# Kernel optimization log

Measured on AMD Instinct MI355X. Metric: run time of the kernel, lower is better.

The kernel has to match this reference:

```python
import jax, jax.numpy as jnp
import numpy as np

D_MODEL = 128
N_HEADS = 8
N_POINTS = 8
MAX_RES = 10.0


def setup_inputs() -> dict:
    key = jax.random.key(0)
    ks = jax.random.split(key, 12)
    B, C, H, W = 4, D_MODEL, 128, 128
    nh, P = N_HEADS, N_POINTS
    inp = {
        'nbr_fea': jax.random.normal(ks[0], (B, C, H, W), jnp.float32),
        'ext_fea': jax.random.normal(ks[1], (B, C, H, W), jnp.float32),
        'flow': jax.random.normal(ks[2], (B, 2, H, W), jnp.float32) * 2.0,
        'W_off': jax.random.normal(ks[3], (C, nh * P * 2), jnp.float32) * 0.02,
        'b_off': jax.random.normal(ks[4], (nh * P * 2,), jnp.float32) * 0.02,
        'W_attn': jax.random.normal(ks[5], (C, nh * P), jnp.float32) * 0.02,
        'b_attn': jnp.zeros((nh * P,), jnp.float32),
        'W_val': jax.random.normal(ks[6], (C, C), jnp.float32) * (1.0 / np.sqrt(C)),
        'b_val': jnp.zeros((C,), jnp.float32),
        'W_out': jax.random.normal(ks[7], (C, C), jnp.float32) * (1.0 / np.sqrt(C)),
        'b_out': jnp.zeros((C,), jnp.float32),
    }
    return inp


def _bilinear_gather(value, loc, H, W):
    # value: (B, nh, HW, dh)  loc: (B, nh, Q, P, 2) normalized to [0,1]
    # grid_sample semantics: align_corners=False, zero padding
    B, nh, HW, dh = value.shape
    Q, P = loc.shape[2], loc.shape[3]
    x = loc[..., 0] * W - 0.5  # (B,nh,Q,P) pixel coords
    y = loc[..., 1] * H - 0.5
    x0 = jnp.floor(x)
    y0 = jnp.floor(y)
    wx = x - x0
    wy = y - y0
    out = jnp.zeros((B, nh, Q * P, dh), value.dtype)
    for dx, dy, wgt in ((0, 0, (1 - wx) * (1 - wy)), (1, 0, wx * (1 - wy)),
                        (0, 1, (1 - wx) * wy), (1, 1, wx * wy)):
        xi = x0 + dx
        yi = y0 + dy
        valid = (xi >= 0) & (xi < W) & (yi >= 0) & (yi < H)
        xi_c = jnp.clip(xi, 0, W - 1).astype(jnp.int32)
        yi_c = jnp.clip(yi, 0, H - 1).astype(jnp.int32)
        idx = (yi_c * W + xi_c).reshape(B, nh, Q * P, 1)
        g = jnp.take_along_axis(value, idx, axis=2)  # (B,nh,QP,dh)
        w_eff = (wgt * valid.astype(value.dtype)).reshape(B, nh, Q * P, 1)
        out = out + g * w_eff
    return out.reshape(B, nh, Q, P, dh)


def reference(nbr_fea, ext_fea, flow, W_off, b_off, W_attn, b_attn, W_val, b_val, W_out, b_out):
    B, C, H, W = nbr_fea.shape
    nh, P = N_HEADS, N_POINTS
    dh = C // nh
    Q = H * W
    # normalized reference points (pixel centers / extent)
    ys = (jnp.arange(H, dtype=jnp.float32) + 0.5) / H
    xs = (jnp.arange(W, dtype=jnp.float32) + 0.5) / W
    yy, xx = jnp.meshgrid(ys, xs, indexing='ij')
    ref = jnp.stack([xx, yy], -1).reshape(Q, 2)  # (Q,2)

    ext = ext_fea.transpose(0, 2, 3, 1).reshape(B, Q, C)
    # flow-guided sampling offsets (pixels), residue bounded by tanh
    off = MAX_RES * jnp.tanh(ext @ W_off + b_off)
    off = off.reshape(B, Q, nh, P, 2)
    flow_q = flow.transpose(0, 2, 3, 1).reshape(B, Q, 1, 1, 2)
    norm = jnp.array([W, H], jnp.float32)
    loc = ref[None, :, None, None, :] + (flow_q + off) / norm  # (B,Q,nh,P,2)

    attn = jax.nn.softmax((ext @ W_attn + b_attn).reshape(B, Q, nh, P), axis=-1)

    val = (nbr_fea.transpose(0, 2, 3, 1).reshape(B, Q, C) @ W_val + b_val)
    val = val.reshape(B, Q, nh, dh).transpose(0, 2, 1, 3)  # (B,nh,HW,dh)

    sampled = _bilinear_gather(val, loc.transpose(0, 2, 1, 3, 4), H, W)  # (B,nh,Q,P,dh)
    agg = jnp.einsum('bnqpd,bqnp->bqnd', sampled, attn).reshape(B, Q, C)
    out = agg @ W_out + b_out  # (B,Q,C)
    return out.reshape(B, H, W, C).transpose(0, 3, 1, 2)
```

## Files before the change

### kernel.cpp

```cpp
#include <hip/hip_runtime.h>
#include <math.h>

namespace {
constexpr int B   = 4;
constexpr int C   = 128;
constexpr int H   = 128;
constexpr int W   = 128;
constexpr int HWn = H * W;
constexpr int NH  = 8;
}

using short8 = __attribute__((ext_vector_type(8))) short;
using f32x4  = __attribute__((ext_vector_type(4))) float;

__device__ __forceinline__ float fast_tanh(float x) {
  float e = __expf(2.f * x);
  return 1.f - 2.f / (e + 1.f);
}
__device__ __forceinline__ unsigned f2bf(float f) {
  unsigned u = __float_as_uint(f);
  return (u + 0x7FFFu + ((u >> 16) & 1u)) >> 16;
}
__device__ __forceinline__ unsigned pack2bf(float a, float b) {
  return f2bf(a) | (f2bf(b) << 16);
}

__global__ __launch_bounds__(256) void prep_weights_kernel(
    const float* __restrict__ Woff, const float* __restrict__ Wattn,
    const float* __restrict__ Wval, const float* __restrict__ Wout,
    unsigned short* __restrict__ wcat_t, unsigned short* __restrict__ wval_t,
    unsigned short* __restrict__ wout_t) {
  int row = blockIdx.x * 256 + threadIdx.x;
  if (row >= 448) return;
  const float* src; int ldn; int col; unsigned short* dst;
  if (row < 192) {
    if (row < 128) { src = Woff; ldn = 128; col = row; }
    else           { src = Wattn; ldn = 64; col = row - 128; }
    dst = wcat_t + row * 128;
  } else if (row < 320) {
    src = Wval; ldn = 128; col = row - 192; dst = wval_t + (row - 192) * 128;
  } else {
    src = Wout; ldn = 128; col = row - 320; dst = wout_t + (row - 320) * 128;
  }
  for (int k0 = 0; k0 < 128; k0 += 8) {
    unsigned pk[4];
#pragma unroll
    for (int j = 0; j < 4; ++j)
      pk[j] = pack2bf(src[(k0 + 2 * j) * ldn + col],
                      src[(k0 + 2 * j + 1) * ldn + col]);
    *(uint4*)(dst + k0) = make_uint4(pk[0], pk[1], pk[2], pk[3]);
  }
}

__global__ __launch_bounds__(256) void gemm_kernel(
    const float* __restrict__ nbr,
    const unsigned short* __restrict__ wval_t,
    const float* __restrict__ bv,
    unsigned short* __restrict__ val) {
  __shared__ unsigned short a_s[64 * 152];
  __shared__ unsigned short b_s[128 * 40];
  const int t    = threadIdx.x;
  const int id   = blockIdx.x;
  const int b    = id >> 8;
  const int q0   = (id & 255) * 64;
  const int wv   = t >> 6;
  const int lane = t & 63;
  const int li   = lane & 15, quad = lane >> 4;

  const float* Ab = nbr + (size_t)b * C * HWn + q0;
#pragma unroll
  for (int it = 0; it < 4; ++it) {
    int idx = t + 256 * it;
    int kp  = idx >> 4;
    int q4  = (idx & 15) * 4;
    float4 fa = *(const float4*)(Ab + (size_t)(2 * kp) * HWn + q4);
    float4 fb = *(const float4*)(Ab + (size_t)(2 * kp + 1) * HWn + q4);
    const float* pa = &fa.x; const float* pb = &fb.x;
#pragma unroll
    for (int j = 0; j < 4; ++j)
      *(unsigned*)&a_s[(q4 + j) * 152 + 2 * kp] = pack2bf(pa[j], pb[j]);
  }

  f32x4 acc[8];
#pragma unroll
  for (int n = 0; n < 8; ++n) acc[n] = (f32x4){0.f, 0.f, 0.f, 0.f};

  for (int ck = 0; ck < 4; ++ck) {
    __syncthreads();
#pragma unroll
    for (int it = 0; it < 2; ++it) {
      int idx = t + 256 * it;
      int n = idx >> 2, seg = idx & 3;
      *(uint4*)&b_s[n * 40 + seg * 8] =
          *(const uint4*)(wval_t + n * 128 + ck * 32 + seg * 8);
    }
    __syncthreads();
    short8 af = *(const short8*)&a_s[(16 * wv + li) * 152 + ck * 32 + quad * 8];
#pragma unroll
    for (int n = 0; n < 8; ++n) {
      short8 bfr = *(const short8*)&b_s[(16 * n + li) * 40 + quad * 8];
      acc[n] = __builtin_amdgcn_mfma_f32_16x16x32_bf16(af, bfr, acc[n], 0, 0, 0);
    }
  }

  __syncthreads();
#pragma unroll
  for (int n = 0; n < 8; ++n) {
    float bias = bv[16 * n + li];
#pragma unroll
    for (int reg = 0; reg < 4; ++reg) {
      int q = 16 * wv + 4 * quad + reg;
      a_s[q * 152 + 16 * n + li] = (unsigned short)f2bf(acc[n][reg] + bias);
    }
  }
  __syncthreads();
  {
    const int qi = t & 63, r = t >> 6;
    uint4 v0 = *(const uint4*)&a_s[qi * 152 + 32 * r];
    uint4 v1 = *(const uint4*)&a_s[qi * 152 + 32 * r + 8];
    uint4 v2 = *(const uint4*)&a_s[qi * 152 + 32 * r + 16];
    uint4 v3 = *(const uint4*)&a_s[qi * 152 + 32 * r + 24];
    unsigned short* d0 = val + ((size_t)(b * NH + 2 * r) * HWn + q0 + qi) * 16;
    unsigned short* d1 = val + ((size_t)(b * NH + 2 * r + 1) * HWn + q0 + qi) * 16;
    *(uint4*)d0 = v0; *(uint4*)(d0 + 8) = v1;
    *(uint4*)d1 = v2; *(uint4*)(d1 + 8) = v3;
  }
}

__global__ __launch_bounds__(256) void gather_out_kernel(
    const float* __restrict__ flow, const float* __restrict__ ext,
    const unsigned short* __restrict__ wcat_t,
    const float* __restrict__ boff, const float* __restrict__ battn,
    const unsigned short* __restrict__ val,
    const unsigned short* __restrict__ wout_t, const float* __restrict__ bout,
    float* __restrict__ out) {
  __shared__ float smem[32 * 200];
  unsigned short* a_ext = (unsigned short*)smem;
  float* l_s = smem;
  unsigned short* a_s2 = (unsigned short*)smem;
  float* c_s = smem;

  const int t  = threadIdx.x;
  const int qi = t & 31;
  const int r  = t >> 5;

  const int blk  = blockIdx.x;
  const int lin  = (blk & 7) * 256 + (blk >> 3);
  const int b    = lin >> 9;
  const int tile = lin & 511;
  const int x0   = (tile & 7) * 16;
  const int y0   = (tile >> 3) * 2;
  const int x    = x0 + (qi & 15);
  const int y    = y0 + (qi >> 4);

  const int lane = t & 63;
  const int li   = lane & 15, quad = lane >> 4;
  const int wv   = t >> 6;

  {
    const float* Eb = ext + (size_t)b * C * HWn;
#pragma unroll
    for (int it = 0; it < 2; ++it) {
      int idx = t + 256 * it;
      int kp  = idx >> 3;
      int pg  = idx & 7;
      int py  = pg >> 2;
      int xo  = (pg & 3) * 4;
      const float* src = Eb + (size_t)(2 * kp) * HWn + (y0 + py) * W + x0 + xo;
      float4 fa = *(const float4*)src;
      float4 fb = *(const float4*)(src + HWn);
      const float* pa = &fa.x; const float* pb = &fb.x;
#pragma unroll
      for (int j = 0; j < 4; ++j)
        *(unsigned*)&a_ext[(pg * 4 + j) * 136 + 2 * kp] = pack2bf(pa[j], pb[j]);
    }
  }
  __syncthreads();

  {
    const int mt   = wv & 1;
    const int nset = wv >> 1;
    f32x4 lacc[6];
#pragma unroll
    for (int i = 0; i < 6; ++i) lacc[i] = (f32x4){0.f, 0.f, 0.f, 0.f};

#pragma unroll 1
    for (int ks = 0; ks < 4; ++ks) {
      short8 af = *(const short8*)&a_ext[(mt * 16 + li) * 136 + ks * 32 + quad * 8];
#pragma unroll
      for (int i = 0; i < 6; ++i) {
        int n = nset * 6 + i;
        short8 bfr = *(const short8*)(wcat_t + (size_t)(16 * n + li) * 128 +
                                      ks * 32 + quad * 8);
        lacc[i] = __builtin_amdgcn_mfma_f32_16x16x32_bf16(af, bfr, lacc[i], 0, 0, 0);
      }
    }
    __syncthreads();

#pragma unroll
    for (int i = 0; i < 6; ++i) {
      int col = 16 * (nset * 6 + i) + li;
      float bias = (col < 128) ? boff[col] : battn[col - 128];
#pragma unroll
      for (int reg = 0; reg < 4; ++reg) {
        int q = mt * 16 + quad * 4 + reg;
        l_s[q * 200 + col] = lacc[i][reg] + bias;
      }
    }
  }
  __syncthreads();

  const float* lrow = l_s + qi * 200;
  float offa[16];
  float atta[8];
#pragma unroll
  for (int j4 = 0; j4 < 4; ++j4) {
    float4 v = *(const float4*)(lrow + 16 * r + 4 * j4);
    offa[4 * j4 + 0] = 10.f * fast_tanh(v.x);
    offa[4 * j4 + 1] = 10.f * fast_tanh(v.y);
    offa[4 * j4 + 2] = 10.f * fast_tanh(v.z);
    offa[4 * j4 + 3] = 10.f * fast_tanh(v.w);
  }
#pragma unroll
  for (int j4 = 0; j4 < 2; ++j4) {
    float4 v = *(const float4*)(lrow + 128 + 8 * r + 4 * j4);
    atta[4 * j4 + 0] = v.x; atta[4 * j4 + 1] = v.y;
    atta[4 * j4 + 2] = v.z; atta[4 * j4 + 3] = v.w;
  }
  {
    float m = atta[0];
#pragma unroll
    for (int p = 1; p < 8; ++p) m = fmaxf(m, atta[p]);
    float s = 0.f;
#pragma unroll
    for (int p = 0; p < 8; ++p) { float ev = __expf(atta[p] - m); atta[p] = ev; s += ev; }
    float inv = 1.f / s;
#pragma unroll
    for (int p = 0; p < 8; ++p) atta[p] *= inv;
  }
  __syncthreads();

  const float xb = (float)x + flow[(size_t)b * 2 * HWn + y * W + x];
  const float yb = (float)y + flow[((size_t)b * 2 + 1) * HWn + y * W + x];

  float agg[16];
#pragma unroll
  for (int j = 0; j < 16; ++j) agg[j] = 0.f;
  const unsigned short* valh =
      val + ((size_t)b * NH + r) * HWn * 16;

#pragma unroll
  for (int p = 0; p < 8; ++p) {
    float sx = xb + offa[2 * p];
    float sy = yb + offa[2 * p + 1];
    float x0f = floorf(sx), y0f = floorf(sy);
    float wx = sx - x0f, wy = sy - y0f;
    int ix0 = (int)x0f, iy0 = (int)y0f;
    int ix1 = ix0 + 1,  iy1 = iy0 + 1;
    float aw  = atta[p];
    float w00 = aw * (1.f - wx) * (1.f - wy);
    float w10 = aw * wx * (1.f - wy);
    float w01 = aw * (1.f - wx) * wy;
    float w11 = aw * wx * wy;
    if ((unsigned)ix0 >= (unsigned)W) { w00 = 0.f; w01 = 0.f; }
    if ((unsigned)ix1 >= (unsigned)W) { w10 = 0.f; w11 = 0.f; }
    if ((unsigned)iy0 >= (unsigned)H) { w00 = 0.f; w10 = 0.f; }
    if ((unsigned)iy1 >= (unsigned)H) { w01 = 0.f; w11 = 0.f; }
    int x0c = min(max(ix0, 0), W - 1);
    int x1c = min(max(ix1, 0), W - 1);
    int y0c = min(max(iy0, 0), H - 1);
    int y1c = min(max(iy1, 0), H - 1);
    const unsigned short* c00 = valh + (size_t)(y0c * W + x0c) * 16;
    const unsigned short* c10 = valh + (size_t)(y0c * W + x1c) * 16;
    const unsigned short* c01 = valh + (size_t)(y1c * W + x0c) * 16;
    const unsigned short* c11 = valh + (size_t)(y1c * W + x1c) * 16;
#pragma unroll
    for (int cn = 0; cn < 4; ++cn) {
      const unsigned short* cp = (cn == 0) ? c00 : (cn == 1) ? c10
                                : (cn == 2) ? c01 : c11;
      float wgt = (cn == 0) ? w00 : (cn == 1) ? w10 : (cn == 2) ? w01 : w11;
      uint4 ga = ((const uint4*)cp)[0];
      uint4 gb = ((const uint4*)cp)[1];
      unsigned gs[8] = {ga.x, ga.y, ga.z, ga.w, gb.x, gb.y, gb.z, gb.w};
#pragma unroll
      for (int i = 0; i < 8; ++i) {
        float lo = __uint_as_float(gs[i] << 16);
        float hi = __uint_as_float(gs[i] & 0xFFFF0000u);
        agg[2 * i]     += wgt * lo;
        agg[2 * i + 1] += wgt * hi;
      }
    }
  }

  {
    unsigned pk[8];
#pragma unroll
    for (int j = 0; j < 8; ++j) pk[j] = pack2bf(agg[2 * j], agg[2 * j + 1]);
    uint4* dst = (uint4*)&a_s2[qi * 136 + 16 * r];
    dst[0] = make_uint4(pk[0], pk[1], pk[2], pk[3]);
    dst[1] = make_uint4(pk[4], pk[5], pk[6], pk[7]);
  }
  __syncthreads();

  const int mt   = wv & 1;
  const int ng   = (wv >> 1) * 4;

  f32x4 acc[4];
#pragma unroll
  for (int i = 0; i < 4; ++i) acc[i] = (f32x4){0.f, 0.f, 0.f, 0.f};

#pragma unroll 1
  for (int ks = 0; ks < 4; ++ks) {
    short8 af = *(const short8*)&a_s2[(mt * 16 + li) * 136 + ks * 32 + quad * 8];
#pragma unroll
    for (int i = 0; i < 4; ++i) {
      short8 bfr = *(const short8*)(wout_t + (size_t)(16 * (ng + i) + li) * 128 +
                                    ks * 32 + quad * 8);
      acc[i] = __builtin_amdgcn_mfma_f32_16x16x32_bf16(af, bfr, acc[i], 0, 0, 0);
    }
  }
  __syncthreads();

#pragma unroll
  for (int i = 0; i < 4; ++i) {
    int c = 16 * (ng + i) + li;
    float bias = bout[c];
#pragma unroll
    for (int reg = 0; reg < 4; ++reg) {
      int q = mt * 16 + quad * 4 + reg;
      c_s[c * 33 + q] = acc[i][reg] + bias;
    }
  }
  __syncthreads();

  float* ob = out + (size_t)b * C * HWn + y * W + x;
#pragma unroll
  for (int j = 0; j < 16; ++j)
    ob[(size_t)(16 * r + j) * HWn] = c_s[(16 * r + j) * 33 + qi];
}

extern "C" void kernel_launch(void* const* d_in, const int* in_sizes, int n_in,
                              void* d_out, int out_size, void* d_ws, size_t ws_size,
                              hipStream_t stream) {
  const float* nbr   = (const float*)d_in[0];
  const float* extf  = (const float*)d_in[1];
  const float* flow  = (const float*)d_in[2];
  const float* Woff  = (const float*)d_in[3];
  const float* boff  = (const float*)d_in[4];
  const float* Wattn = (const float*)d_in[5];
  const float* battn = (const float*)d_in[6];
  const float* Wval  = (const float*)d_in[7];
  const float* bval  = (const float*)d_in[8];
  const float* Wout  = (const float*)d_in[9];
  const float* bout  = (const float*)d_in[10];
  float* outp = (float*)d_out;

  unsigned short* val    = (unsigned short*)d_ws;
  unsigned short* wcat_t = val + (size_t)B * NH * HWn * 16;
  unsigned short* wval_t = wcat_t + 192 * 128;
  unsigned short* wout_t = wval_t + 128 * 128;

  prep_weights_kernel<<<dim3(2), dim3(256), 0, stream>>>(
      Woff, Wattn, Wval, Wout, wcat_t, wval_t, wout_t);
  gemm_kernel<<<dim3(1024), dim3(256), 0, stream>>>(
      nbr, wval_t, bval, val);
  gather_out_kernel<<<dim3(2048), dim3(256), 0, stream>>>(
      flow, extf, wcat_t, boff, battn, val, wout_t, bout, outp);
}
```

Before: 228.7 us.

## Halve value-projection GEMM tile and read weight fragments directly from global

```diff
diff --git a/kernel.cpp b/kernel.cpp
--- a/kernel.cpp
+++ b/kernel.cpp
@@ -57,22 +57,21 @@
     const unsigned short* __restrict__ wval_t,
     const float* __restrict__ bv,
     unsigned short* __restrict__ val) {
-  __shared__ unsigned short a_s[64 * 152];
-  __shared__ unsigned short b_s[128 * 40];
+  __shared__ unsigned short a_s[32 * 152];
   const int t    = threadIdx.x;
   const int id   = blockIdx.x;
-  const int b    = id >> 8;
-  const int q0   = (id & 255) * 64;
+  const int b    = id >> 9;
+  const int q0   = (id & 511) * 32;
   const int wv   = t >> 6;
   const int lane = t & 63;
   const int li   = lane & 15, quad = lane >> 4;
 
   const float* Ab = nbr + (size_t)b * C * HWn + q0;
 #pragma unroll
-  for (int it = 0; it < 4; ++it) {
+  for (int it = 0; it < 2; ++it) {
     int idx = t + 256 * it;
-    int kp  = idx >> 4;
-    int q4  = (idx & 15) * 4;
+    int kp  = idx >> 3;
+    int q4  = (idx & 7) * 4;
     float4 fa = *(const float4*)(Ab + (size_t)(2 * kp) * HWn + q4);
     float4 fb = *(const float4*)(Ab + (size_t)(2 * kp + 1) * HWn + q4);
     const float* pa = &fa.x; const float* pb = &fb.x;
@@ -80,50 +79,44 @@
     for (int j = 0; j < 4; ++j)
       *(unsigned*)&a_s[(q4 + j) * 152 + 2 * kp] = pack2bf(pa[j], pb[j]);
   }
-
-  f32x4 acc[8];
-#pragma unroll
-  for (int n = 0; n < 8; ++n) acc[n] = (f32x4){0.f, 0.f, 0.f, 0.f};
-
+  __syncthreads();
+
+  const int mt = wv & 1;
+  const int ng = (wv >> 1) * 4;
+  f32x4 acc[4];
+#pragma unroll
+  for (int i = 0; i < 4; ++i) acc[i] = (f32x4){0.f, 0.f, 0.f, 0.f};
+
+#pragma unroll 1
   for (int ck = 0; ck < 4; ++ck) {
-    __syncthreads();
-#pragma unroll
-    for (int it = 0; it < 2; ++it) {
-      int idx = t + 256 * it;
-      int n = idx >> 2, seg = idx & 3;
-      *(uint4*)&b_s[n * 40 + seg * 8] =
-          *(const uint4*)(wval_t + n * 128 + ck * 32 + seg * 8);
-    }
-    __syncthreads();
-    short8 af = *(const short8*)&a_s[(16 * wv + li) * 152 + ck * 32 + quad * 8];
-#pragma unroll
-    for (int n = 0; n < 8; ++n) {
-      short8 bfr = *(const short8*)&b_s[(16 * n + li) * 40 + quad * 8];
-      acc[n] = __builtin_amdgcn_mfma_f32_16x16x32_bf16(af, bfr, acc[n], 0, 0, 0);
-    }
-  }
-
-  __syncthreads();
-#pragma unroll
-  for (int n = 0; n < 8; ++n) {
-    float bias = bv[16 * n + li];
+    short8 af = *(const short8*)&a_s[(16 * mt + li) * 152 + ck * 32 + quad * 8];
+#pragma unroll
+    for (int i = 0; i < 4; ++i) {
+      short8 bfr = *(const short8*)(wval_t + (size_t)(16 * (ng + i) + li) * 128 +
+                                    ck * 32 + quad * 8);
+      acc[i] = __builtin_amdgcn_mfma_f32_16x16x32_bf16(af, bfr, acc[i], 0, 0, 0);
+    }
+  }
+  __syncthreads();
+
+#pragma unroll
+  for (int i = 0; i < 4; ++i) {
+    int c = 16 * (ng + i) + li;
+    float bias = bv[c];
 #pragma unroll
     for (int reg = 0; reg < 4; ++reg) {
-      int q = 16 * wv + 4 * quad + reg;
-      a_s[q * 152 + 16 * n + li] = (unsigned short)f2bf(acc[n][reg] + bias);
-    }
-  }
-  __syncthreads();
-  {
-    const int qi = t & 63, r = t >> 6;
-    uint4 v0 = *(const uint4*)&a_s[qi * 152 + 32 * r];
-    uint4 v1 = *(const uint4*)&a_s[qi * 152 + 32 * r + 8];
-    uint4 v2 = *(const uint4*)&a_s[qi * 152 + 32 * r + 16];
-    uint4 v3 = *(const uint4*)&a_s[qi * 152 + 32 * r + 24];
-    unsigned short* d0 = val + ((size_t)(b * NH + 2 * r) * HWn + q0 + qi) * 16;
-    unsigned short* d1 = val + ((size_t)(b * NH + 2 * r + 1) * HWn + q0 + qi) * 16;
-    *(uint4*)d0 = v0; *(uint4*)(d0 + 8) = v1;
-    *(uint4*)d1 = v2; *(uint4*)(d1 + 8) = v3;
+      int q = mt * 16 + quad * 4 + reg;
+      a_s[q * 152 + c] = (unsigned short)f2bf(acc[i][reg] + bias);
+    }
+  }
+  __syncthreads();
+
+  {
+    const int qi = t & 31, hs = t >> 5;
+    uint4 v0 = *(const uint4*)&a_s[qi * 152 + 16 * hs];
+    uint4 v1 = *(const uint4*)&a_s[qi * 152 + 16 * hs + 8];
+    unsigned short* d = val + ((size_t)(b * NH + hs) * HWn + q0 + qi) * 16;
+    *(uint4*)d = v0; *(uint4*)(d + 8) = v1;
   }
 }
 
@@ -134,7 +127,7 @@
     const unsigned short* __restrict__ val,
     const unsigned short* __restrict__ wout_t, const float* __restrict__ bout,
     float* __restrict__ out) {
-  __shared__ float smem[32 * 200];
+  __shared__ float smem[32 * 196];
   unsigned short* a_ext = (unsigned short*)smem;
   float* l_s = smem;
   unsigned short* a_s2 = (unsigned short*)smem;
@@ -204,13 +197,13 @@
 #pragma unroll
       for (int reg = 0; reg < 4; ++reg) {
         int q = mt * 16 + quad * 4 + reg;
-        l_s[q * 200 + col] = lacc[i][reg] + bias;
+        l_s[q * 196 + col] = lacc[i][reg] + bias;
       }
     }
   }
   __syncthreads();
 
-  const float* lrow = l_s + qi * 200;
+  const float* lrow = l_s + qi * 196;
   float offa[16];
   float atta[8];
 #pragma unroll
@@ -362,7 +355,7 @@
 
   prep_weights_kernel<<<dim3(2), dim3(256), 0, stream>>>(
       Woff, Wattn, Wval, Wout, wcat_t, wval_t, wout_t);
-  gemm_kernel<<<dim3(1024), dim3(256), 0, stream>>>(
+  gemm_kernel<<<dim3(2048), dim3(256), 0, stream>>>(
       nbr, wval_t, bval, val);
   gather_out_kernel<<<dim3(2048), dim3(256), 0, stream>>>(
       flow, extf, wcat_t, boff, battn, val, wout_t, bout, outp);
```

Measured after the change: 237.7 us. 1.04x slower.
